# Kernel tuning notes

Hardware: AMD Instinct MI355X
Metric: run time of the kernel (lower is better)

The kernel has to match this reference:

```python
import jax, jax.numpy as jnp
import numpy as np

B, F, D, H = 16384, 10, 512, 8
DH = D // H
EPS = 1e-5


def setup_inputs() -> dict:
    key = jax.random.key(0)
    ks = jax.random.split(key, 12)
    s = 1.0 / np.sqrt(D)
    inp = {
        "x": jax.random.normal(ks[0], (B, F), dtype=jnp.float32),
        # per-feature Linear(1, D): weight (F, D), bias (F, D)
        "Wf": jax.random.normal(ks[1], (F, D), dtype=jnp.float32) * 1.0,
        "bf": jax.random.normal(ks[2], (F, D), dtype=jnp.float32) * 0.1,
        # MHA in/out projections (torch layout: out_features x in_features)
        "Wq": jax.random.normal(ks[3], (D, D), dtype=jnp.float32) * s,
        "Wk": jax.random.normal(ks[4], (D, D), dtype=jnp.float32) * s,
        "Wv": jax.random.normal(ks[5], (D, D), dtype=jnp.float32) * s,
        "bq": jax.random.normal(ks[6], (D,), dtype=jnp.float32) * 0.02,
        "bk": jax.random.normal(ks[7], (D,), dtype=jnp.float32) * 0.02,
        "bv": jax.random.normal(ks[8], (D,), dtype=jnp.float32) * 0.02,
        "Wo": jax.random.normal(ks[9], (D, D), dtype=jnp.float32) * s,
        "bo": jax.random.normal(ks[10], (D,), dtype=jnp.float32) * 0.02,
        "gamma": jnp.ones((D,), dtype=jnp.float32),
        "beta": jnp.zeros((D,), dtype=jnp.float32),
    }
    return inp


def reference(x, Wf, bf, Wq, Wk, Wv, bq, bk, bv, Wo, bo, gamma, beta):
    # Fused per-feature scalar Linear + ReLU: (B,F,1)*(F,D) + (F,D) -> (B,F,D)
    p = jax.nn.relu(x[:, :, None] * Wf[None] + bf[None])
    # Multi-head self-attention (q = k = v = p), torch Linear: y = x @ W.T + b
    def heads(t):  # (B,F,D) -> (B,H,F,DH)
        return t.reshape(B, F, H, DH).transpose(0, 2, 1, 3)
    q = heads(p @ Wq.T + bq)
    k = heads(p @ Wk.T + bk)
    v = heads(p @ Wv.T + bv)
    scores = jnp.einsum("bhqd,bhkd->bhqk", q, k) / jnp.sqrt(jnp.float32(DH))
    attn = jax.nn.softmax(scores, axis=-1)
    o = jnp.einsum("bhqk,bhkd->bhqd", attn, v)
    o = o.transpose(0, 2, 1, 3).reshape(B, F, D) @ Wo.T + bo
    # LayerNorm over last dim
    mu = jnp.mean(o, axis=-1, keepdims=True)
    var = jnp.mean(jnp.square(o - mu), axis=-1, keepdims=True)
    ln = (o - mu) * jax.lax.rsqrt(var + EPS) * gamma + beta
    # sum pool over the function/sequence axis
    return jnp.sum(ln, axis=1)  # (B, D)
```

## Files before the change

kernel.cpp:

```cpp
#include <hip/hip_runtime.h>
#include <stdint.h>


typedef __bf16 bf16;
typedef __bf16 bf16x8 __attribute__((ext_vector_type(8)));
typedef float f32x4 __attribute__((ext_vector_type(4)));

#define EPS 1e-5f

static constexpr size_t O_ELEMS   = (size_t)16384 * 10 * 512;
static constexpr size_t O_BYTES   = O_ELEMS * 2;
static constexpr size_t WQKV_BYTES = (size_t)8 * 192 * 512 * 2;

__device__ __forceinline__ void async_copy16(void* lds, const void* g) {
  __builtin_amdgcn_global_load_lds(
      (const __attribute__((address_space(1))) uint32_t*)g,
      (__attribute__((address_space(3))) uint32_t*)lds, 16, 0, 0);
}

__global__ __launch_bounds__(256) void pack_weights(
    const float* __restrict__ Wq, const float* __restrict__ Wk,
    const float* __restrict__ Wv, const float* __restrict__ Wo,
    bf16* __restrict__ wqkv, bf16* __restrict__ wob) {
  int idx = blockIdx.x * 256 + threadIdx.x;
#pragma unroll
  for (int u = 0; u < 4; ++u) {
    int i = idx + u * 262144;
    if (i < 786432) {
      int pr = i >> 9, k = i & 511;
      int h = pr / 192, w = pr - h * 192;
      int t = w >> 6, r = w & 63;
      const float* src = (t == 0) ? Wq : ((t == 1) ? Wk : Wv);
      wqkv[i] = (bf16)src[(h * 64 + r) * 512 + k];
    } else {
      int j = i - 786432;
      wob[j] = (bf16)Wo[j];
    }
  }
}

__global__ __launch_bounds__(512, 2) void kern_fused(
    const float* __restrict__ x, const float* __restrict__ Wf,
    const float* __restrict__ bfv, const bf16* __restrict__ wqkv,
    const float* __restrict__ bq, const float* __restrict__ bk,
    const float* __restrict__ bv, bf16* __restrict__ O,
    const bf16* __restrict__ wob, const float* __restrict__ bo,
    const float* __restrict__ gamma, const float* __restrict__ beta,
    float* __restrict__ out) {
  __shared__ __align__(16) char smem[153600];
  char* sA  = smem;
  char* sB0 = smem + 81920;
  char* sB1 = smem + 106496;
  char* sQK = smem + 131072;
  bf16* vbuf = (bf16*)sB1;
  float* scp = (float*)(sB1 + 10240);

  const int tid = threadIdx.x;
  const int wave = tid >> 6;
  const int lane = tid & 63;
  const int lm = lane & 15;
  const int lg = lane >> 4;
  const int wm = wave >> 2;
  const int wn = wave & 3;
  const int b0 = blockIdx.x * 8;
  const int lr = lane >> 3;
  const int kcg = (lane & 7) ^ lr;
  const int x7 = lm & 7;

#pragma unroll
  for (int jb = 0; jb < 3; ++jb) {
    int rb = wave + 8 * jb;
    async_copy16(sB0 + rb * 1024, wqkv + (size_t)(rb * 8 + lr) * 512 + kcg * 8);
  }

#pragma unroll
  for (int it = 0; it < 10; ++it) {
    int c = tid + it * 512;
    int s = c / 640, rem = c - s * 640;
    int r = rem >> 3, kcp = rem & 7;
    int kc = kcp ^ (r & 7);
    int k = s * 64 + kc * 8;
    int bl = r / 10, f = r - bl * 10;
    float xv = x[(b0 + bl) * 10 + f];
    const float* wf = Wf + f * 512 + k;
    const float* bp = bfv + f * 512 + k;
    bf16x8 pv;
#pragma unroll
    for (int j = 0; j < 8; ++j) pv[j] = (bf16)fmaxf(xv * wf[j] + bp[j], 0.f);
    *(bf16x8*)(sA + s * 10240 + r * 128 + kcp * 16) = pv;
  }
  __syncthreads();

  bf16x8 af[2][3];
#pragma unroll
  for (int kk = 0; kk < 2; ++kk)
#pragma unroll
    for (int mt = 0; mt < 3; ++mt)
      if (mt < 2 || wm == 0) {
        int m = wm * 48 + mt * 16 + lm;
        af[kk][mt] = *(const bf16x8*)(sA + m * 128 + (((kk * 4 + lg) ^ x7) << 4));
      }

  for (int h = 0; h < 8; ++h) {
    f32x4 acc[3][3];
#pragma unroll
    for (int i = 0; i < 3; ++i)
#pragma unroll
      for (int j = 0; j < 3; ++j) { f32x4 z = {0.f, 0.f, 0.f, 0.f}; acc[i][j] = z; }

    for (int s = 0; s < 8; ++s) {
      int t = h * 8 + s;
      char* bufC = (s & 1) ? sB1 : sB0;
      char* bufN = (s & 1) ? sB0 : sB1;
      if (t != 63) {
        int tn = t + 1;
        int h2 = tn >> 3, s2 = tn & 7;
        const bf16* srcb = wqkv + (size_t)h2 * 98304 + s2 * 64 + kcg * 8;
#pragma unroll
        for (int jb = 0; jb < 3; ++jb) {
          int rb = wave + 8 * jb;
          async_copy16(bufN + rb * 1024, srcb + (size_t)(rb * 8 + lr) * 512);
        }
      }
#pragma unroll
      for (int kk = 0; kk < 2; ++kk) {
        int ch = ((kk * 4 + lg) ^ x7) << 4;
        bf16x8 bfr[3];
#pragma unroll
        for (int nt = 0; nt < 3; ++nt) {
          int n = wn * 48 + nt * 16 + lm;
          bfr[nt] = *(const bf16x8*)(bufC + n * 128 + ch);
        }
        __builtin_amdgcn_s_setprio(1);
#pragma unroll
        for (int mt = 0; mt < 3; ++mt)
          if (mt < 2 || wm == 0)
#pragma unroll
            for (int nt = 0; nt < 3; ++nt)
              acc[mt][nt] = __builtin_amdgcn_mfma_f32_16x16x32_bf16(af[kk][mt], bfr[nt], acc[mt][nt], 0, 0, 0);
        __builtin_amdgcn_s_setprio(0);
      }
      {
        const char* sAn = sA + ((s + 1) & 7) * 10240;
#pragma unroll
        for (int kk = 0; kk < 2; ++kk)
#pragma unroll
          for (int mt = 0; mt < 3; ++mt)
            if (mt < 2 || wm == 0) {
              int m = wm * 48 + mt * 16 + lm;
              af[kk][mt] = *(const bf16x8*)(sAn + m * 128 + (((kk * 4 + lg) ^ x7) << 4));
            }
      }
      __syncthreads();
    }

    {
      float bias[3];
#pragma unroll
      for (int nt = 0; nt < 3; ++nt) {
        int col = wn * 48 + nt * 16 + lm;
        bias[nt] = (col < 64) ? bq[h * 64 + col]
                 : (col < 128) ? bk[h * 64 + col - 64]
                 : bv[h * 64 + col - 128];
      }
#pragma unroll
      for (int mt = 0; mt < 3; ++mt) {
        int rowb = wm * 48 + mt * 16 + lg * 4;
        if (rowb < 80) {
#pragma unroll
          for (int r = 0; r < 4; ++r) {
            int rw = rowb + r;
#pragma unroll
            for (int nt = 0; nt < 3; ++nt) {
              int col = wn * 48 + nt * 16 + lm;
              float val = acc[mt][nt][r] + bias[nt];
              if (col < 128)
                *(bf16*)(sQK + rw * 256 + (((col >> 3) ^ (rw & 7)) << 4) + (col & 7) * 2) = (bf16)val;
              else
                vbuf[rw * 64 + (col - 128)] = (bf16)val;
            }
          }
        }
      }
    }
    __syncthreads();

    {
      const int b = wave;
      f32x4 sv = {0.f, 0.f, 0.f, 0.f};
      const int rowa = b * 10 + lm;
      const int x7r = rowa & 7;
#pragma unroll
      for (int kk = 0; kk < 2; ++kk) {
        bf16x8 qf = *(const bf16x8*)(sQK + rowa * 256 + (((kk * 4 + lg) ^ x7r) << 4));
        bf16x8 kf = *(const bf16x8*)(sQK + rowa * 256 + (((8 + kk * 4 + lg) ^ x7r) << 4));
        sv = __builtin_amdgcn_mfma_f32_16x16x32_bf16(qf, kf, sv, 0, 0, 0);
      }
#pragma unroll
      for (int r = 0; r < 4; ++r) {
        float val = (lm < 10) ? sv[r] * 0.125f : -1e30f;
        float mx = val;
#pragma unroll
        for (int off = 1; off < 16; off <<= 1) mx = fmaxf(mx, __shfl_xor(mx, off));
        float e = __expf(val - mx);
        float ssum = e;
#pragma unroll
        for (int off = 1; off < 16; off <<= 1) ssum += __shfl_xor(ssum, off);
        int i = lg * 4 + r;
        if (i < 10 && lm < 12) scp[(b * 10 + i) * 12 + lm] = e / ssum;
      }
    }

    {
      const int b = wave;
      const int d = lane;
      float vv[10];
#pragma unroll
      for (int j = 0; j < 10; ++j) vv[j] = (float)vbuf[(b * 10 + j) * 64 + d];
      bf16* Ob = O + ((size_t)(b0 + b) * 10) * 512 + h * 64 + d;
#pragma unroll
      for (int i = 0; i < 10; ++i) {
        const float* ar = scp + (b * 10 + i) * 12;
        f32x4 a0 = *(const f32x4*)ar;
        f32x4 a1 = *(const f32x4*)(ar + 4);
        float o = a0[0] * vv[0] + a0[1] * vv[1] + a0[2] * vv[2] + a0[3] * vv[3]
                + a1[0] * vv[4] + a1[1] * vv[5] + a1[2] * vv[6] + a1[3] * vv[7]
                + ar[8] * vv[8] + ar[9] * vv[9];
        Ob[(size_t)i * 512] = (bf16)o;
      }
    }
    __syncthreads();
  }

  {
    char* Ab = smem;
    char* Bb = smem + 12288;
    float* partial = (float*)(smem + 145920);
    float* stats   = (float*)(smem + 148992);
    const bf16* Osrc = O + (size_t)blockIdx.x * 80 * 512;

    f32x4 acc[3][8];
#pragma unroll
    for (int i = 0; i < 3; ++i)
#pragma unroll
      for (int j = 0; j < 8; ++j) { f32x4 z = {0.f, 0.f, 0.f, 0.f}; acc[i][j] = z; }

    for (int s = 0; s < 8; ++s) {
      async_copy16(Ab + wave * 1024, Osrc + (size_t)(wave * 8 + lr) * 512 + s * 64 + kcg * 8);
      if (wave < 2) {
        int rb2 = 8 + wave;
        async_copy16(Ab + rb2 * 1024, Osrc + (size_t)(rb2 * 8 + lr) * 512 + s * 64 + kcg * 8);
      }
#pragma unroll
      for (int jb = 0; jb < 8; ++jb) {
        int rb = wave + 8 * jb;
        async_copy16(Bb + rb * 1024, wob + (size_t)(rb * 8 + lr) * 512 + s * 64 + kcg * 8);
      }
      __syncthreads();
#pragma unroll
      for (int kk = 0; kk < 2; ++kk) {
        int ch = ((kk * 4 + lg) ^ x7) << 4;
        bf16x8 a2[3], b2[8];
#pragma unroll
        for (int mt = 0; mt < 3; ++mt)
          if (mt < 2 || wm == 0)
            a2[mt] = *(const bf16x8*)(Ab + (wm * 48 + mt * 16 + lm) * 128 + ch);
#pragma unroll
        for (int nt = 0; nt < 8; ++nt)
          b2[nt] = *(const bf16x8*)(Bb + (wn * 128 + nt * 16 + lm) * 128 + ch);
        __builtin_amdgcn_s_setprio(1);
#pragma unroll
        for (int mt = 0; mt < 3; ++mt)
          if (mt < 2 || wm == 0)
#pragma unroll
            for (int nt = 0; nt < 8; ++nt)
              acc[mt][nt] = __builtin_amdgcn_mfma_f32_16x16x32_bf16(a2[mt], b2[nt], acc[mt][nt], 0, 0, 0);
        __builtin_amdgcn_s_setprio(0);
      }
      __syncthreads();
    }

#pragma unroll
    for (int nt = 0; nt < 8; ++nt) {
      float bb = bo[wn * 128 + nt * 16 + lm];
#pragma unroll
      for (int mt = 0; mt < 3; ++mt)
#pragma unroll
        for (int r = 0; r < 4; ++r) acc[mt][nt][r] += bb;
    }

#pragma unroll
    for (int mt = 0; mt < 3; ++mt)
#pragma unroll
      for (int r = 0; r < 4; ++r) {
        float s1 = 0.f, s2 = 0.f;
#pragma unroll
        for (int nt = 0; nt < 8; ++nt) { float v = acc[mt][nt][r]; s1 += v; s2 += v * v; }
#pragma unroll
        for (int off = 1; off < 16; off <<= 1) {
          s1 += __shfl_xor(s1, off);
          s2 += __shfl_xor(s2, off);
        }
        if (lm == 0) {
          int row = wm * 48 + mt * 16 + lg * 4 + r;
          if (row < 80) {
            partial[(row * 4 + wn) * 2]     = s1;
            partial[(row * 4 + wn) * 2 + 1] = s2;
          }
        }
      }
    __syncthreads();
    if (tid < 80) {
      float s1 = 0.f, s2 = 0.f;
#pragma unroll
      for (int w = 0; w < 4; ++w) {
        s1 += partial[(tid * 4 + w) * 2];
        s2 += partial[(tid * 4 + w) * 2 + 1];
      }
      float mu = s1 * (1.f / 512.f);
      float var = s2 * (1.f / 512.f) - mu * mu;
      stats[tid * 2]     = mu;
      stats[tid * 2 + 1] = rsqrtf(var + EPS);
    }
    __syncthreads();
    bf16* lnb = (bf16*)smem;
#pragma unroll
    for (int mt = 0; mt < 3; ++mt)
#pragma unroll
      for (int r = 0; r < 4; ++r) {
        int row = wm * 48 + mt * 16 + lg * 4 + r;
        if (row < 80) {
          float mu = stats[row * 2], rr = stats[row * 2 + 1];
#pragma unroll
          for (int nt = 0; nt < 8; ++nt) {
            int col = wn * 128 + nt * 16 + lm;
            lnb[row * 520 + col] = (bf16)((acc[mt][nt][r] - mu) * rr);
          }
        }
      }
    __syncthreads();
#pragma unroll
    for (int u = 0; u < 8; ++u) {
      int id = tid + u * 512;
      int b = id >> 9, n = id & 511;
      float ssum = 0.f;
#pragma unroll
      for (int f = 0; f < 10; ++f) ssum += (float)lnb[(b * 10 + f) * 520 + n];
      out[((size_t)blockIdx.x * 8 + b) * 512 + n] = gamma[n] * ssum + 10.f * beta[n];
    }
  }
}

extern "C" void kernel_launch(void* const* d_in, const int* in_sizes, int n_in,
                              void* d_out, int out_size, void* d_ws, size_t ws_size,
                              hipStream_t stream) {
  const float* x     = (const float*)d_in[0];
  const float* Wf    = (const float*)d_in[1];
  const float* bfv   = (const float*)d_in[2];
  const float* Wq    = (const float*)d_in[3];
  const float* Wk    = (const float*)d_in[4];
  const float* Wv    = (const float*)d_in[5];
  const float* bq    = (const float*)d_in[6];
  const float* bk    = (const float*)d_in[7];
  const float* bv    = (const float*)d_in[8];
  const float* Wo    = (const float*)d_in[9];
  const float* bo    = (const float*)d_in[10];
  const float* gamma = (const float*)d_in[11];
  const float* beta  = (const float*)d_in[12];
  float* out = (float*)d_out;

  char* ws = (char*)d_ws;
  bf16* O    = (bf16*)ws;
  bf16* wqkv = (bf16*)(ws + O_BYTES);
  bf16* wob  = (bf16*)(ws + O_BYTES + WQKV_BYTES);

  pack_weights<<<1024, 256, 0, stream>>>(Wq, Wk, Wv, Wo, wqkv, wob);
  kern_fused<<<2048, 512, 0, stream>>>(x, Wf, bfv, wqkv, bq, bk, bv, O,
                                       wob, bo, gamma, beta, out);
}
```

Baseline: 755.8 us.

## Double-buffer output-projection GEMM and use explicit waitcnt barriers in QKV loop

In the QKV projection loop, A fragments are now loaded from LDS per k-step rather than prefetched across iterations. The buffer parity now uses the global step index, and __syncthreads is replaced by explicit vmcnt/lgkmcnt waits plus raw s_barrier, so in-flight async weight copies overlap compute. The output-projection stage goes from single-buffered 8 steps of K=64 to double-buffered 16 steps of K=32, with a new swizzled LDS layout, so global-to-LDS copies of O and Wo overlap the MFMAs. This adds hand-counted waitcnt values that must match the number of outstanding loads per wave, which is fragile.

Result: faster. 709.2 us (-6.2%).

```diff
diff --git a/kernel.cpp b/kernel.cpp
--- a/kernel.cpp
+++ b/kernel.cpp
@@ -91,16 +91,6 @@
   }
   __syncthreads();
 
-  bf16x8 af[2][3];
-#pragma unroll
-  for (int kk = 0; kk < 2; ++kk)
-#pragma unroll
-    for (int mt = 0; mt < 3; ++mt)
-      if (mt < 2 || wm == 0) {
-        int m = wm * 48 + mt * 16 + lm;
-        af[kk][mt] = *(const bf16x8*)(sA + m * 128 + (((kk * 4 + lg) ^ x7) << 4));
-      }
-
   for (int h = 0; h < 8; ++h) {
     f32x4 acc[3][3];
 #pragma unroll
@@ -110,8 +100,8 @@
 
     for (int s = 0; s < 8; ++s) {
       int t = h * 8 + s;
-      char* bufC = (s & 1) ? sB1 : sB0;
-      char* bufN = (s & 1) ? sB0 : sB1;
+      char* bufC = (t & 1) ? sB1 : sB0;
+      char* bufN = (t & 1) ? sB0 : sB1;
       if (t != 63) {
         int tn = t + 1;
         int h2 = tn >> 3, s2 = tn & 7;
@@ -121,37 +111,37 @@
           int rb = wave + 8 * jb;
           async_copy16(bufN + rb * 1024, srcb + (size_t)(rb * 8 + lr) * 512);
         }
-      }
+        asm volatile("s_waitcnt vmcnt(3)" ::: "memory");
+      } else {
+        asm volatile("s_waitcnt vmcnt(0)" ::: "memory");
+      }
+      __builtin_amdgcn_sched_barrier(0);
+      __builtin_amdgcn_s_barrier();
+      __builtin_amdgcn_sched_barrier(0);
 #pragma unroll
       for (int kk = 0; kk < 2; ++kk) {
         int ch = ((kk * 4 + lg) ^ x7) << 4;
-        bf16x8 bfr[3];
-#pragma unroll
-        for (int nt = 0; nt < 3; ++nt) {
-          int n = wn * 48 + nt * 16 + lm;
-          bfr[nt] = *(const bf16x8*)(bufC + n * 128 + ch);
-        }
-        __builtin_amdgcn_s_setprio(1);
+        bf16x8 af[3], bfr[3];
 #pragma unroll
         for (int mt = 0; mt < 3; ++mt)
           if (mt < 2 || wm == 0)
+            af[mt] = *(const bf16x8*)(sA + s * 10240 + (wm * 48 + mt * 16 + lm) * 128 + ch);
+#pragma unroll
+        for (int nt = 0; nt < 3; ++nt)
+          bfr[nt] = *(const bf16x8*)(bufC + (wn * 48 + nt * 16 + lm) * 128 + ch);
+        __builtin_amdgcn_s_setprio(1);
+#pragma unroll
+        for (int mt = 0; mt < 3; ++mt)
+          if (mt < 2 || wm == 0)
 #pragma unroll
             for (int nt = 0; nt < 3; ++nt)
-              acc[mt][nt] = __builtin_amdgcn_mfma_f32_16x16x32_bf16(af[kk][mt], bfr[nt], acc[mt][nt], 0, 0, 0);
+              acc[mt][nt] = __builtin_amdgcn_mfma_f32_16x16x32_bf16(af[mt], bfr[nt], acc[mt][nt], 0, 0, 0);
         __builtin_amdgcn_s_setprio(0);
       }
-      {
-        const char* sAn = sA + ((s + 1) & 7) * 10240;
-#pragma unroll
-        for (int kk = 0; kk < 2; ++kk)
-#pragma unroll
-          for (int mt = 0; mt < 3; ++mt)
-            if (mt < 2 || wm == 0) {
-              int m = wm * 48 + mt * 16 + lm;
-              af[kk][mt] = *(const bf16x8*)(sAn + m * 128 + (((kk * 4 + lg) ^ x7) << 4));
-            }
-      }
-      __syncthreads();
+      asm volatile("s_waitcnt lgkmcnt(0)" ::: "memory");
+      __builtin_amdgcn_sched_barrier(0);
+      __builtin_amdgcn_s_barrier();
+      __builtin_amdgcn_sched_barrier(0);
     }
 
     {
@@ -233,11 +223,17 @@
   }
 
   {
-    char* Ab = smem;
-    char* Bb = smem + 12288;
+    char* Ab0 = smem;
+    char* Ab1 = smem + 5120;
+    char* Bb0 = smem + 10240;
+    char* Bb1 = smem + 43008;
     float* partial = (float*)(smem + 145920);
     float* stats   = (float*)(smem + 148992);
-    const bf16* Osrc = O + (size_t)blockIdx.x * 80 * 512;
+    const char* Ob = (const char*)(O + (size_t)blockIdx.x * 80 * 512);
+    const char* Wb = (const char*)wob;
+
+    const int srow  = lane >> 2;
+    const int sgran = (lane & 3) ^ ((lane >> 3) & 3);
 
     f32x4 acc[3][8];
 #pragma unroll
@@ -245,39 +241,63 @@
 #pragma unroll
       for (int j = 0; j < 8; ++j) { f32x4 z = {0.f, 0.f, 0.f, 0.f}; acc[i][j] = z; }
 
-    for (int s = 0; s < 8; ++s) {
-      async_copy16(Ab + wave * 1024, Osrc + (size_t)(wave * 8 + lr) * 512 + s * 64 + kcg * 8);
-      if (wave < 2) {
-        int rb2 = 8 + wave;
-        async_copy16(Ab + rb2 * 1024, Osrc + (size_t)(rb2 * 8 + lr) * 512 + s * 64 + kcg * 8);
-      }
-#pragma unroll
-      for (int jb = 0; jb < 8; ++jb) {
-        int rb = wave + 8 * jb;
-        async_copy16(Bb + rb * 1024, wob + (size_t)(rb * 8 + lr) * 512 + s * 64 + kcg * 8);
-      }
-      __syncthreads();
-#pragma unroll
-      for (int kk = 0; kk < 2; ++kk) {
-        int ch = ((kk * 4 + lg) ^ x7) << 4;
-        bf16x8 a2[3], b2[8];
-#pragma unroll
-        for (int mt = 0; mt < 3; ++mt)
-          if (mt < 2 || wm == 0)
-            a2[mt] = *(const bf16x8*)(Ab + (wm * 48 + mt * 16 + lm) * 128 + ch);
-#pragma unroll
-        for (int nt = 0; nt < 8; ++nt)
-          b2[nt] = *(const bf16x8*)(Bb + (wn * 128 + nt * 16 + lm) * 128 + ch);
-        __builtin_amdgcn_s_setprio(1);
-#pragma unroll
-        for (int mt = 0; mt < 3; ++mt)
-          if (mt < 2 || wm == 0)
-#pragma unroll
-            for (int nt = 0; nt < 8; ++nt)
-              acc[mt][nt] = __builtin_amdgcn_mfma_f32_16x16x32_bf16(a2[mt], b2[nt], acc[mt][nt], 0, 0, 0);
-        __builtin_amdgcn_s_setprio(0);
-      }
-      __syncthreads();
+#define STAGE2(AbN, BbN, s_)                                                     \
+    {                                                                            \
+      size_t co = (size_t)(s_) * 64 + sgran * 16;                                \
+      _Pragma("unroll")                                                          \
+      for (int j = 0; j < 4; ++j) {                                              \
+        int R0 = (wave * 4 + j) * 16;                                            \
+        async_copy16((BbN) + R0 * 64, Wb + (size_t)(R0 + srow) * 1024 + co);     \
+      }                                                                          \
+      if (wave < 5) {                                                            \
+        int R0 = wave * 16;                                                      \
+        async_copy16((AbN) + R0 * 64, Ob + (size_t)(R0 + srow) * 1024 + co);     \
+      }                                                                          \
+    }
+
+    STAGE2(Ab0, Bb0, 0);
+
+    for (int s = 0; s < 16; ++s) {
+      char* AbC = (s & 1) ? Ab1 : Ab0;
+      char* BbC = (s & 1) ? Bb1 : Bb0;
+      char* AbN = (s & 1) ? Ab0 : Ab1;
+      char* BbN = (s & 1) ? Bb0 : Bb1;
+      if (s != 15) {
+        STAGE2(AbN, BbN, s + 1);
+        if (wave < 5) asm volatile("s_waitcnt vmcnt(5)" ::: "memory");
+        else          asm volatile("s_waitcnt vmcnt(4)" ::: "memory");
+      } else {
+        asm volatile("s_waitcnt vmcnt(0)" ::: "memory");
+      }
+      __builtin_amdgcn_sched_barrier(0);
+      __builtin_amdgcn_s_barrier();
+      __builtin_amdgcn_sched_barrier(0);
+
+      bf16x8 a2[3], b2[8];
+#pragma unroll
+      for (int mt = 0; mt < 3; ++mt)
+        if (mt < 2 || wm == 0) {
+          int m = wm * 48 + mt * 16 + lm;
+          a2[mt] = *(const bf16x8*)(AbC + (m >> 1) * 128 + (m & 1) * 64 + (((lg ^ ((m >> 1) & 3))) << 4));
+        }
+#pragma unroll
+      for (int nt = 0; nt < 8; ++nt) {
+        int n = wn * 128 + nt * 16 + lm;
+        b2[nt] = *(const bf16x8*)(BbC + (n >> 1) * 128 + (n & 1) * 64 + (((lg ^ ((n >> 1) & 3))) << 4));
+      }
+      __builtin_amdgcn_s_setprio(1);
+#pragma unroll
+      for (int mt = 0; mt < 3; ++mt)
+        if (mt < 2 || wm == 0)
+#pragma unroll
+          for (int nt = 0; nt < 8; ++nt)
+            acc[mt][nt] = __builtin_amdgcn_mfma_f32_16x16x32_bf16(a2[mt], b2[nt], acc[mt][nt], 0, 0, 0);
+      __builtin_amdgcn_s_setprio(0);
+
+      asm volatile("s_waitcnt lgkmcnt(0)" ::: "memory");
+      __builtin_amdgcn_sched_barrier(0);
+      __builtin_amdgcn_s_barrier();
+      __builtin_amdgcn_sched_barrier(0);
     }
 
 #pragma unroll
@@ -349,6 +369,7 @@
       out[((size_t)blockIdx.x * 8 + b) * 512 + n] = gamma[n] * ssum + 10.f * beta[n];
     }
   }
+#undef STAGE2
 }
 
 extern "C" void kernel_launch(void* const* d_in, const int* in_sizes, int n_in,
```
